# Optimization experiments

Measured on AMD Instinct MI355X. Metric: run time of the kernel, lower is better.

The kernel has to match this reference:

```python
import jax, jax.numpy as jnp
import numpy as np
from jax import lax

KS = 10      # kernel_size (asserted == 10 in the torch module)
DCT_N = 10   # dct_n


def _dct_pair(N):
    k = np.arange(N)[:, None]
    i = np.arange(N)[None, :]
    w = np.full((N, 1), np.sqrt(2.0 / N))
    w[0, 0] = np.sqrt(1.0 / N)
    d = w * np.cos(np.pi * (i + 0.5) * k / N)
    return jnp.asarray(d, jnp.float32), jnp.asarray(np.linalg.inv(d), jnp.float32)


def _conv1d(x, w):
    # x: [B, C, L], w: [O, C, K], VALID conv (bias=False in torch)
    return lax.conv_general_dilated(x, w, (1,), 'VALID',
                                    dimension_numbers=('NCH', 'OIH', 'NCH'))


def _two_conv(x, w1, w2):
    return jax.nn.relu(_conv1d(jax.nn.relu(_conv1d(x, w1)), w2))


def _gconv(x, w, att, b):
    # GraphConvolution: att @ (x @ w) + b ; x: [B, node, f_in]
    return jnp.einsum('nm,bmo->bno', att, jnp.einsum('bmf,fo->bmo', x, w)) + b


def _gcn(x, gc1_w, gc1_att, gc1_b, gcb_w, gcb_att, gcb_b, gc7_w, gc7_att, gc7_b):
    # Standard motion-prediction GCN (eval mode: BN=identity, dropout off)
    y = jnp.tanh(_gconv(x, gc1_w, gc1_att, gc1_b))
    for s in range(gcb_w.shape[0]):  # small fixed num_stage
        h = jnp.tanh(_gconv(y, gcb_w[s, 0], gcb_att[s, 0], gcb_b[s, 0]))
        h = jnp.tanh(_gconv(h, gcb_w[s, 1], gcb_att[s, 1], gcb_b[s, 1]))
        y = y + h
    return _gconv(y, gc7_w, gc7_att, gc7_b) + x


def _ffc(x, wl, wg):
    # RealFFC(dim=3): spectral branch (rFFT over time, 1x1 conv on real/imag,
    # ReLU, irFFT) + local 1x1 branch. x: [B, 3, F/3, T]
    y = jnp.fft.rfft(x, axis=-1)
    yc = jnp.concatenate([y.real, y.imag], axis=1)            # [B, 6, F/3, K]
    yc = jax.nn.relu(jnp.einsum('oc,bcfk->bofk', wg, yc))
    re, im = jnp.split(yc, 2, axis=1)
    spec = jnp.fft.irfft(re + 1j * im, n=x.shape[-1], axis=-1)
    return jnp.einsum('oc,bcft->boft', wl, x) + spec


def _forward(input_seq, wq1, wq2, wk1, wk2,
             gc1_w, gc1_att, gc1_b, gcb_w, gcb_att, gcb_b,
             gc7_w, gc7_att, gc7_b, mlp_w1, mlp_w2, ffc_wl, ffc_wg,
             output_n, input_n):
    seq = input_seq[:, :input_n]
    B, _, F = seq.shape
    blen = KS + output_n                       # DCT block length (30)
    dctm, idctm = _dct_pair(blen)
    key_seq = jnp.swapaxes(seq, 1, 2)[:, :, :input_n - output_n]
    query_seq = jnp.swapaxes(seq, 1, 2)[:, :, -KS:]
    # im2col-style overlapping temporal blocks -> per-block DCT
    nvb = input_n - blen + 1
    idx = np.arange(blen)[None, :] + np.arange(nvb)[:, None]
    blocks = seq[:, idx]                       # [B, nvb, blen, F]
    # matches torch reshape(...,dct_n,-1).transpose(2,3).reshape: feature-major
    dvb = jnp.einsum('dk,bnkf->bnfd', dctm[:DCT_N], blocks).reshape(B, nvb, -1)
    key_feat = _two_conv(key_seq / 1000.0, wk1, wk2)       # [B, D, nvb]
    query_feat = _two_conv(query_seq / 1000.0, wq1, wq2)   # [B, D, 1]
    score = jnp.einsum('bdq,bdk->bqk', query_feat, key_feat) + 1e-15
    attn = score / jnp.sum(score, axis=2, keepdims=True)   # sum-normalized attention
    attended = jnp.einsum('bqk,bkf->bqf', attn, dvb)[:, 0].reshape(B, F, DCT_N)
    # FFC branch: pad with last frame x10, fold F into (3, F//3)
    ffc_in = jnp.concatenate([seq, jnp.repeat(seq[:, -1:], 10, axis=1)], axis=1)
    ffc_in = jnp.swapaxes(ffc_in, 1, 2).reshape(B, 3, F // 3, input_n + 10)
    ffc_out = _ffc(ffc_in, ffc_wl, ffc_wg).reshape(B, F, input_n + 10)[:, :, :DCT_N]
    ffc_out = jnp.swapaxes(ffc_out, 1, 2)      # [B, DCT_N, F]
    # GCN branch: last KS frames + last frame repeated output_n times
    gidx = np.concatenate([np.arange(input_n - KS, input_n),
                           np.full(output_n, input_n - 1)])
    gcn_in = seq[:, gidx]                      # [B, blen, F]
    dct_in = jnp.einsum('dk,bkf->bfd', dctm[:DCT_N], gcn_in)
    gcn_out = _gcn(dct_in, gc1_w, gc1_att, gc1_b, gcb_w, gcb_att, gcb_b,
                   gc7_w, gc7_att, gc7_b)      # [B, F, DCT_N]
    combined = jnp.concatenate([gcn_out, attended], axis=-1)
    recon = jnp.einsum('kd,bfd->bkf', idctm[:, :DCT_N], combined[:, :, :DCT_N])  # [B, blen, F]
    fused = jnp.swapaxes(jnp.concatenate([recon, ffc_out], axis=1), 1, 2)  # [B, F, blen+DCT_N=40]
    h = jax.nn.relu(jnp.einsum('bft,ot->bfo', fused, mlp_w1))  # Linear(40,256), no bias
    out = jnp.einsum('bfo,to->bft', h, mlp_w2)                 # Linear(256,40), no bias
    out = jnp.swapaxes(out, 1, 2)[:, :DCT_N]   # [B, DCT_N, F]
    return out[:, :, None, :]                  # [B, DCT_N, itera=1, F]


def setup_inputs() -> dict:
    key = jax.random.key(0)
    ks = jax.random.split(key, 20)
    B, T, F, D, NS = 1024, 50, 48, 512, 2
    p = lambda k, shp: jax.random.normal(k, shp, dtype=jnp.float32) * 0.05
    return {
        'input_seq': jax.random.normal(ks[0], (B, T, F), dtype=jnp.float32),
        'wq1': p(ks[1], (D, F, 6)), 'wq2': p(ks[2], (D, D, 5)),
        'wk1': p(ks[3], (D, F, 6)), 'wk2': p(ks[4], (D, D, 5)),
        'gc1_w': p(ks[5], (10, D)), 'gc1_att': p(ks[6], (F, F)), 'gc1_b': p(ks[7], (D,)),
        'gcb_w': p(ks[8], (NS, 2, D, D)), 'gcb_att': p(ks[9], (NS, 2, F, F)),
        'gcb_b': p(ks[10], (NS, 2, D)),
        'gc7_w': p(ks[11], (D, 10)), 'gc7_att': p(ks[12], (F, F)), 'gc7_b': p(ks[13], (10,)),
        'mlp_w1': p(ks[14], (256, 40)), 'mlp_w2': p(ks[15], (40, 256)),
        'ffc_wl': p(ks[16], (3, 3)), 'ffc_wg': p(ks[17], (6, 6)),
        'output_n': 20, 'input_n': 50, 'itera': 1,
    }


def reference(input_seq, wq1, wq2, wk1, wk2, gc1_w, gc1_att, gc1_b,
              gcb_w, gcb_att, gcb_b, gc7_w, gc7_att, gc7_b,
              mlp_w1, mlp_w2, ffc_wl, ffc_wg, output_n, input_n, itera):
    assert itera == 1  # single-iteration path (the torch itera>1 branch is skipped)
    return _forward(input_seq, wq1, wq2, wk1, wk2,
                    gc1_w, gc1_att, gc1_b, gcb_w, gcb_att, gcb_b,
                    gc7_w, gc7_att, gc7_b, mlp_w1, mlp_w2, ffc_wl, ffc_wg,
                    output_n, input_n)
```

## Files before the change

### kernel.cpp

```cpp
#include <hip/hip_runtime.h>
#include <math.h>

#define BB 1024
#define TT 50
#define FF 48
#define EXTN 60
#define NFREQ 31

typedef _Float16 h8 __attribute__((ext_vector_type(8)));
typedef _Float16 h4 __attribute__((ext_vector_type(4)));
typedef float f4 __attribute__((ext_vector_type(4)));

__device__ __forceinline__ float fast_tanh(float x) {
    float e = __expf(2.0f * x);
    return 1.0f - 2.0f * __builtin_amdgcn_rcpf(e + 1.0f);
}

__global__ void prep_kernel(const float* __restrict__ gcb_w, _Float16* __restrict__ P,
                            const float* __restrict__ gc1_w, _Float16* __restrict__ P1,
                            const float* __restrict__ gc7_w, _Float16* __restrict__ P7,
                            const float* __restrict__ mlp_w1, _Float16* __restrict__ Pw1,
                            const float* __restrict__ mlp_w2, _Float16* __restrict__ Pw2,
                            const float* __restrict__ gc1_att, const float* __restrict__ gcb_att,
                            const float* __restrict__ gc7_att, _Float16* __restrict__ attp,
                            float* __restrict__ dctm, float* __restrict__ dtail) {
    int blk = blockIdx.x, tid = threadIdx.x;
    const _Float16 HZ = (_Float16)0.0f;
    if (blk < 512) {
        int z = blk >> 7;
        int idx = ((blk & 127) << 8) | tid;
        int lane = idx & 63, t8 = idx >> 6;
        int nt = t8 & 7, kw = t8 >> 3;
        int ks = kw & 15, wv = kw >> 4;
        int n = wv * 128 + nt * 16 + (lane & 15);
        int k0 = ks * 32 + (lane >> 4) * 8;
        const float* src = gcb_w + (size_t)z * 262144 + n;
        h8 v;
        #pragma unroll
        for (int j = 0; j < 8; ++j) v[j] = (_Float16)src[(size_t)(k0 + j) * 512];
        *(h8*)(P + (size_t)z * 262144 + (size_t)idx * 8) = v;
    } else if (blk < 528) {
        int idx = ((blk - 512) << 8) | tid;
        int lane = idx & 63, t8 = idx >> 6;
        int nt = t8 & 7, kw = t8 >> 3;
        int ks = kw & 1, wv = kw >> 1;
        int n = wv * 128 + nt * 16 + (lane & 15);
        int k0 = ks * 32 + (lane >> 4) * 8;
        h8 v;
        #pragma unroll
        for (int j = 0; j < 8; ++j) v[j] = (k0 + j < 10) ? (_Float16)gc1_w[(k0 + j) * 512 + n] : HZ;
        *(h8*)(P1 + (size_t)idx * 8) = v;
    } else if (blk < 532) {
        int idx = ((blk - 528) << 8) | tid;
        int lane = idx & 63, t8 = idx >> 6;
        int ks = t8 & 3, wv = t8 >> 2;
        int n = lane & 15;
        int k0 = wv * 128 + ks * 32 + (lane >> 4) * 8;
        h8 v;
        #pragma unroll
        for (int j = 0; j < 8; ++j) v[j] = (n < 10) ? (_Float16)gc7_w[(k0 + j) * 10 + n] : HZ;
        *(h8*)(P7 + (size_t)idx * 8) = v;
    } else if (blk < 540) {
        int idx = ((blk - 532) << 8) | tid;
        int lane = idx & 63, t8 = idx >> 6;
        int ks = t8 & 1, q = t8 >> 1;
        int nt = q & 3, wv = q >> 2;
        int o = wv * 64 + nt * 16 + (lane & 15);
        int k0 = ks * 32 + (lane >> 4) * 8;
        h8 v;
        #pragma unroll
        for (int j = 0; j < 8; ++j) v[j] = (k0 + j < 40) ? (_Float16)mlp_w1[o * 40 + k0 + j] : HZ;
        *(h8*)(Pw1 + (size_t)idx * 8) = v;
    } else if (blk < 542) {
        int idx = ((blk - 540) << 8) | tid;
        int lane = idx & 63, ks = idx >> 6;
        int m = lane & 15;
        int k0 = ks * 32 + (lane >> 4) * 8;
        h8 v;
        #pragma unroll
        for (int j = 0; j < 8; ++j) v[j] = (m < 10) ? (_Float16)mlp_w2[m * 256 + k0 + j] : HZ;
        *(h8*)(Pw2 + (size_t)idx * 8) = v;
    } else if (blk < 614) {
        int idx = (blk - 542) * 256 + tid;
        if (idx < 18432) {
            int l = idx / 3072, r = (idx % 3072) / 64, m = idx & 63;
            float v = 0.f;
            if (m < 48) {
                v = (l == 0) ? gc1_att[r * 48 + m]
                  : (l <= 4) ? gcb_att[(l - 1) * 2304 + r * 48 + m]
                             : gc7_att[r * 48 + m];
            }
            attp[idx] = (_Float16)v;
        }
    } else {
        int idx = (blk - 614) * 256 + tid;
        if (idx < 900) {
            int d = idx / 30, k = idx % 30;
            double w = (d == 0) ? sqrt(1.0 / 30.0) : sqrt(2.0 / 30.0);
            dctm[idx] = (float)(w * cos(M_PI * (k + 0.5) * d / 30.0));
        } else if (idx < 910) {
            int d = idx - 900;
            double w = (d == 0) ? sqrt(1.0 / 30.0) : sqrt(2.0 / 30.0);
            double s = 0.0;
            for (int k = 10; k < 30; ++k) s += w * cos(M_PI * (k + 0.5) * d / 30.0);
            dtail[d] = (float)s;
        }
    }
}

template<int KSTEPS, int MODE>
__device__ __forceinline__ void gcn_layer(char* S, char* T,
        const _Float16* __restrict__ Pw, const _Float16* __restrict__ attp,
        const float* __restrict__ bias, h4* sv,
        int lane, int wv, int l16, int quad) {
    h8 ab[3][2];
    #pragma unroll
    for (int it = 0; it < 3; ++it)
        #pragma unroll
        for (int ks = 0; ks < 2; ++ks)
            ab[it][ks] = *(const h8*)(attp + (it * 16 + l16) * 64 + ks * 32 + quad * 8);

    f4 acc[3][8];
    #pragma unroll
    for (int mt = 0; mt < 3; ++mt)
        #pragma unroll
        for (int nt = 0; nt < 8; ++nt) acc[mt][nt] = (f4)0.0f;

    const _Float16* Pb = Pw + (size_t)wv * (KSTEPS * 8 * 512) + lane * 8;
    __syncthreads();
    const int xm = l16 & 7;
    #pragma unroll 2
    for (int ks = 0; ks < KSTEPS; ++ks) {
        h8 a[3], bfr[8];
        #pragma unroll
        for (int nt = 0; nt < 8; ++nt)
            bfr[nt] = *(const h8*)(Pb + (ks * 8 + nt) * 512);
        #pragma unroll
        for (int mt = 0; mt < 3; ++mt)
            a[mt] = *(h8*)(S + (mt * 16 + l16) * 1024 + (((ks * 4 + quad) ^ xm) << 4));
        #pragma unroll
        for (int mt = 0; mt < 3; ++mt)
            #pragma unroll
            for (int nt = 0; nt < 8; ++nt)
                acc[mt][nt] = __builtin_amdgcn_mfma_f32_16x16x32_f16(a[mt], bfr[nt], acc[mt][nt], 0, 0, 0);
    }
    __syncthreads();

    if (lane < 48) {
        int row = lane / 3, s = lane % 3;
        *(h8*)(T + row * 144 + 96 + s * 16) = (h8)(_Float16)0.0f;
    }

    #pragma unroll
    for (int nt = 0; nt < 8; ++nt) {
        #pragma unroll
        for (int mt = 0; mt < 3; ++mt) {
            h4 hv;
            #pragma unroll
            for (int j = 0; j < 4; ++j) hv[j] = (_Float16)acc[mt][nt][j];
            *(h4*)(T + l16 * 144 + (mt * 16 + quad * 4) * 2) = hv;
        }
        asm volatile("s_waitcnt lgkmcnt(0)" ::: "memory");
        h8 tf0 = *(h8*)(T + l16 * 144 + quad * 16);
        h8 tf1 = *(h8*)(T + l16 * 144 + 64 + quad * 16);
        f4 acc2[3];
        #pragma unroll
        for (int it = 0; it < 3; ++it) {
            acc2[it] = __builtin_amdgcn_mfma_f32_16x16x32_f16(tf0, ab[it][0], (f4)0.0f, 0, 0, 0);
            acc2[it] = __builtin_amdgcn_mfma_f32_16x16x32_f16(tf1, ab[it][1], acc2[it], 0, 0, 0);
        }
        const int c0 = wv * 128 + nt * 16 + quad * 4;
        const f4 bv = *(const f4*)(bias + c0);
        #pragma unroll
        for (int it = 0; it < 3; ++it) {
            int f = it * 16 + l16;
            char* sp = S + f * 1024 + (((c0 >> 3) ^ (f & 7)) << 4) + ((c0 & 7) << 1);
            if (MODE == 1) sv[nt * 3 + it] = *(h4*)sp;
            h4 o;
            #pragma unroll
            for (int j = 0; j < 4; ++j) {
                float v = fast_tanh(acc2[it][j] + bv[j]);
                if (MODE == 2) v += (float)sv[nt * 3 + it][j];
                o[j] = (_Float16)v;
            }
            *(h4*)sp = o;
        }
    }
}

__launch_bounds__(256, 2)
__global__ void gcn_fused_kernel(const float* __restrict__ seq,
                                 const _Float16* __restrict__ P1,
                                 const _Float16* __restrict__ Pm,
                                 const _Float16* __restrict__ P7,
                                 const _Float16* __restrict__ attp,
                                 const float* __restrict__ gc1_b,
                                 const float* __restrict__ gcb_b,
                                 const float* __restrict__ gc7_b,
                                 const float* __restrict__ dctm,
                                 const float* __restrict__ dtail,
                                 float* __restrict__ fusedb) {
    __shared__ __align__(16) char smem[63744];
    char* S    = smem;
    char* R    = smem + 49152;
    char* dctf = smem + 61440;
    const int tid = threadIdx.x, lane = tid & 63, wv = tid >> 6;
    const int l16 = lane & 15, quad = lane >> 4;
    const int b = blockIdx.x;
    char* T = R + wv * 2304;

    if (tid < 120) *(f4*)(R + tid * 16) = *(const f4*)(seq + (size_t)b * 2400 + 1920 + tid * 4);
    for (int v = tid; v < 310; v += 256)
        ((float*)(R + 2048))[v] = (v < 300) ? dctm[v] : dtail[v - 300];
    __syncthreads();
    for (int v = tid; v < 480; v += 256) {
        int f = v / 10, d = v % 10;
        const float* q = (const float*)R;
        const float* L = (const float*)(R + 2048);
        float a = L[300 + d] * q[9 * 48 + f];
        #pragma unroll
        for (int k = 0; k < 10; ++k) a += L[d * 30 + k] * q[k * 48 + f];
        ((float*)dctf)[f * 12 + d] = a;
    }
    __syncthreads();
    for (int v = tid; v < 384; v += 256) {
        int m = v >> 3, g = v & 7;
        h8 w = (h8)(_Float16)0.0f;
        if (g < 2) {
            #pragma unroll
            for (int j = 0; j < 8; ++j) {
                int d = g * 8 + j;
                if (d < 10) w[j] = (_Float16)((float*)dctf)[m * 12 + d];
            }
        }
        *(h8*)(S + m * 1024 + ((g ^ (m & 7)) << 4)) = w;
    }

    h4 sv[24];
    gcn_layer<2, 0>(S, T, P1,          attp,          gc1_b,        sv, lane, wv, l16, quad);
    gcn_layer<16, 1>(S, T, Pm,          attp + 3072,  gcb_b,        sv, lane, wv, l16, quad);
    gcn_layer<16, 2>(S, T, Pm + 262144, attp + 6144,  gcb_b + 512,  sv, lane, wv, l16, quad);
    gcn_layer<16, 1>(S, T, Pm + 524288, attp + 9216,  gcb_b + 1024, sv, lane, wv, l16, quad);
    gcn_layer<16, 2>(S, T, Pm + 786432, attp + 12288, gcb_b + 1536, sv, lane, wv, l16, quad);

    __syncthreads();
    {
        f4 acc[3];
        #pragma unroll
        for (int mt = 0; mt < 3; ++mt) acc[mt] = (f4)0.0f;
        const _Float16* Pb7 = P7 + wv * 2048 + lane * 8;
        #pragma unroll
        for (int ks = 0; ks < 4; ++ks) {
            h8 bfr = *(const h8*)(Pb7 + ks * 512);
            int kh = wv * 128 + ks * 32;
            #pragma unroll
            for (int mt = 0; mt < 3; ++mt) {
                h8 a = *(h8*)(S + (mt * 16 + l16) * 1024 + ((((kh >> 3) + quad) ^ (l16 & 7)) << 4));
                acc[mt] = __builtin_amdgcn_mfma_f32_16x16x32_f16(a, bfr, acc[mt], 0, 0, 0);
            }
        }
        #pragma unroll
        for (int mt = 0; mt < 3; ++mt)
            *(f4*)(R + wv * 3072 + l16 * 192 + (mt * 16 + quad * 4) * 4) = acc[mt];
    }
    __syncthreads();
    if (wv == 0) {
        h4 tw[3]; int ns[3], ms[3];
        #pragma unroll
        for (int q = 0; q < 3; ++q) {
            int idx = lane * 3 + q;
            int n = idx / 12, m0 = (idx % 12) * 4;
            f4 s = *(f4*)(R + n * 192 + m0 * 4);
            s += *(f4*)(R + 3072 + n * 192 + m0 * 4);
            s += *(f4*)(R + 6144 + n * 192 + m0 * 4);
            s += *(f4*)(R + 9216 + n * 192 + m0 * 4);
            h4 h;
            #pragma unroll
            for (int j = 0; j < 4; ++j) h[j] = (_Float16)s[j];
            tw[q] = h; ns[q] = n; ms[q] = m0;
        }
        asm volatile("s_waitcnt lgkmcnt(0)" ::: "memory");
        #pragma unroll
        for (int q = 0; q < 3; ++q) *(h4*)(R + ns[q] * 144 + ms[q] * 2) = tw[q];
        if (lane < 48) {
            int row = lane / 3, s2 = lane % 3;
            *(h8*)(R + row * 144 + 96 + s2 * 16) = (h8)(_Float16)0.0f;
        }
        asm volatile("s_waitcnt lgkmcnt(0)" ::: "memory");
        h8 tf0 = *(h8*)(R + l16 * 144 + quad * 16);
        h8 tf1 = *(h8*)(R + l16 * 144 + 64 + quad * 16);
        const _Float16* a7 = attp + 15360;
        f4 acc2[3];
        #pragma unroll
        for (int it = 0; it < 3; ++it) {
            h8 ab0 = *(const h8*)(a7 + (it * 16 + l16) * 64 + quad * 8);
            h8 ab1 = *(const h8*)(a7 + (it * 16 + l16) * 64 + 32 + quad * 8);
            acc2[it] = __builtin_amdgcn_mfma_f32_16x16x32_f16(tf0, ab0, (f4)0.0f, 0, 0, 0);
            acc2[it] = __builtin_amdgcn_mfma_f32_16x16x32_f16(tf1, ab1, acc2[it], 0, 0, 0);
        }
        char* G = R + 4096;
        #pragma unroll
        for (int it = 0; it < 3; ++it) {
            int f = it * 16 + l16;
            #pragma unroll
            for (int j = 0; j < 4; ++j) {
                int c = quad * 4 + j;
                if (c < 10) {
                    float v = acc2[it][j] + gc7_b[c] + ((float*)dctf)[f * 12 + c];
                    *(float*)(G + f * 64 + c * 4) = v;
                }
            }
        }
    }
    __syncthreads();
    {
        char* G = R + 4096;
        for (int v = tid; v < 1440; v += 256) {
            int f = v / 30, t = v % 30;
            float s = 0.f;
            #pragma unroll
            for (int d = 0; d < 10; ++d) s += dctm[d * 30 + t] * *(float*)(G + f * 64 + d * 4);
            fusedb[(size_t)b * 1440 + v] = s;
        }
    }
}

__launch_bounds__(256, 3)
__global__ void ffc_mlp_kernel(const float* __restrict__ seq,
                               const float* __restrict__ fusedb,
                               const float* __restrict__ wl,
                               const float* __restrict__ wg,
                               const _Float16* __restrict__ Pw1,
                               const _Float16* __restrict__ Pw2,
                               float* __restrict__ out) {
    __shared__ __align__(16) char smem[45312];
    float* ext = (float*)smem;
    float* Xre = (float*)(smem + 11520);
    float* Xim = (float*)(smem + 17664);
    float* Yo  = (float*)(smem + 23808);
    _Float16* hlds = (_Float16*)smem;
    char* R2 = smem + 25344;
    _Float16* fus = (_Float16*)(smem + 37632);
    float* c60 = (float*)(smem + 44544);
    float* s60 = (float*)(smem + 44784);
    float* wls = (float*)(smem + 45024);
    float* wgs = (float*)(smem + 45072);

    const int b = blockIdx.x, tid = threadIdx.x;
    const int lane = tid & 63, wv = tid >> 6;
    const int l16 = lane & 15, quad = lane >> 4;
    const float* s = seq + (size_t)b * TT * FF;

    for (int idx = tid; idx < EXTN * FF; idx += 256) {
        int t = idx / FF, f = idx % FF;
        int ts = t < TT ? t : TT - 1;
        ext[t * FF + f] = s[ts * FF + f];
    }
    if (tid < 60) { c60[tid] = cospif(tid / 30.0f); s60[tid] = sinpif(tid / 30.0f); }
    if (tid >= 64 && tid < 73) wls[tid - 64] = wl[tid - 64];
    if (tid >= 128 && tid < 164) wgs[tid - 128] = wg[tid - 128];
    __syncthreads();
    for (int idx = tid; idx < FF * NFREQ; idx += 256) {
        int f = idx % FF, k = idx / FF;
        float re = 0.f, im = 0.f;
        int kt = 0;
        for (int t = 0; t < EXTN; ++t) {
            float v = ext[t * FF + f];
            re += v * c60[kt];
            im -= v * s60[kt];
            kt += k; kt = (kt >= 60) ? kt - 60 : kt;
        }
        Xre[f * 32 + k] = re; Xim[f * 32 + k] = im;
    }
    __syncthreads();
    for (int idx = tid; idx < 6 * 16 * NFREQ; idx += 256) {
        int k = idx % NFREQ; int g = (idx / NFREQ) % 16; int o = idx / (NFREQ * 16);
        float v = wgs[o * 6 + 0] * Xre[g * 32 + k]        + wgs[o * 6 + 1] * Xre[(16 + g) * 32 + k]
                + wgs[o * 6 + 2] * Xre[(32 + g) * 32 + k] + wgs[o * 6 + 3] * Xim[g * 32 + k]
                + wgs[o * 6 + 4] * Xim[(16 + g) * 32 + k] + wgs[o * 6 + 5] * Xim[(32 + g) * 32 + k];
        Yo[(o * 16 + g) * 32 + k] = fmaxf(v, 0.f);
    }
    __syncthreads();
    for (int v = tid; v < 1440; v += 256) {
        int f = v / 30, t = v % 30;
        fus[f * 72 + t] = (_Float16)fusedb[(size_t)b * 1440 + v];
    }
    for (int v = tid; v < 1152; v += 256) {
        int f = v / 24, t = 40 + v % 24;
        fus[f * 72 + t] = (_Float16)0.0f;
    }
    for (int idx = tid; idx < 480; idx += 256) {
        int t = idx % 10; int g = (idx / 10) % 16; int c = idx / 160;
        float acc = Yo[(c * 16 + g) * 32 + 0] + Yo[(c * 16 + g) * 32 + 30] * ((t & 1) ? -1.f : 1.f);
        float s2 = 0.f;
        int kt = t;
        for (int k = 1; k < 30; ++k) {
            s2 += Yo[(c * 16 + g) * 32 + k] * c60[kt] - Yo[((c + 3) * 16 + g) * 32 + k] * s60[kt];
            kt += t; kt = (kt >= 60) ? kt - 60 : kt;
        }
        acc = (acc + 2.f * s2) * (1.0f / 60.0f);
        float loc = wls[c * 3 + 0] * ext[t * FF + g] + wls[c * 3 + 1] * ext[t * FF + 16 + g]
                  + wls[c * 3 + 2] * ext[t * FF + 32 + g];
        int f = c * 16 + g;
        fus[f * 72 + 30 + t] = (_Float16)(acc + loc);
    }
    __syncthreads();
    f4 acc1[3][4];
    #pragma unroll
    for (int mt = 0; mt < 3; ++mt)
        #pragma unroll
        for (int nt = 0; nt < 4; ++nt) acc1[mt][nt] = (f4)0.0f;
    #pragma unroll
    for (int ks = 0; ks < 2; ++ks) {
        h8 af[3], bf[4];
        #pragma unroll
        for (int mt = 0; mt < 3; ++mt)
            af[mt] = *(h8*)((char*)fus + (mt * 16 + l16) * 144 + ks * 64 + quad * 16);
        #pragma unroll
        for (int nt = 0; nt < 4; ++nt)
            bf[nt] = *(const h8*)(Pw1 + (size_t)(((wv * 4 + nt) * 2 + ks) * 512) + lane * 8);
        #pragma unroll
        for (int mt = 0; mt < 3; ++mt)
            #pragma unroll
            for (int nt = 0; nt < 4; ++nt)
                acc1[mt][nt] = __builtin_amdgcn_mfma_f32_16x16x32_f16(af[mt], bf[nt], acc1[mt][nt], 0, 0, 0);
    }
    __syncthreads();
    #pragma unroll
    for (int mt = 0; mt < 3; ++mt)
        #pragma unroll
        for (int nt = 0; nt < 4; ++nt) {
            int o = wv * 64 + nt * 16 + l16;
            #pragma unroll
            for (int j = 0; j < 4; ++j) {
                int f = mt * 16 + quad * 4 + j;
                hlds[f * 264 + o] = (_Float16)fmaxf(acc1[mt][nt][j], 0.f);
            }
        }
    __syncthreads();
    f4 acc2[3];
    #pragma unroll
    for (int nt3 = 0; nt3 < 3; ++nt3) acc2[nt3] = (f4)0.0f;
    #pragma unroll
    for (int ss = 0; ss < 2; ++ss) {
        int ks = wv * 2 + ss;
        h8 aw = *(const h8*)(Pw2 + (size_t)ks * 512 + lane * 8);
        #pragma unroll
        for (int nt3 = 0; nt3 < 3; ++nt3) {
            h8 bh = *(h8*)((char*)hlds + (nt3 * 16 + l16) * 528 + ks * 64 + quad * 16);
            acc2[nt3] = __builtin_amdgcn_mfma_f32_16x16x32_f16(aw, bh, acc2[nt3], 0, 0, 0);
        }
    }
    #pragma unroll
    for (int nt3 = 0; nt3 < 3; ++nt3)
        *(f4*)(R2 + wv * 3072 + (nt3 * 16 + l16) * 64 + quad * 16) = acc2[nt3];
    __syncthreads();
    for (int v = tid; v < 768; v += 256) {
        int f = v >> 4, t = v & 15;
        float sm = 0.f;
        #pragma unroll
        for (int w4 = 0; w4 < 4; ++w4) sm += *(float*)(R2 + w4 * 3072 + f * 64 + t * 4);
        if (t < 10) out[(size_t)b * 480 + t * 48 + f] = sm;
    }
}

extern "C" void kernel_launch(void* const* d_in, const int* in_sizes, int n_in,
                              void* d_out, int out_size, void* d_ws, size_t ws_size,
                              hipStream_t stream) {
    (void)in_sizes; (void)n_in; (void)out_size;
    const float* seq     = (const float*)d_in[0];
    const float* gc1_w   = (const float*)d_in[5];
    const float* gc1_att = (const float*)d_in[6];
    const float* gc1_b   = (const float*)d_in[7];
    const float* gcb_w   = (const float*)d_in[8];
    const float* gcb_att = (const float*)d_in[9];
    const float* gcb_b   = (const float*)d_in[10];
    const float* gc7_w   = (const float*)d_in[11];
    const float* gc7_att = (const float*)d_in[12];
    const float* gc7_b   = (const float*)d_in[13];
    const float* mlp_w1  = (const float*)d_in[14];
    const float* mlp_w2  = (const float*)d_in[15];
    const float* ffc_wl  = (const float*)d_in[16];
    const float* ffc_wg  = (const float*)d_in[17];
    float* out = (float*)d_out;
    char* ws = (char*)d_ws;

    float*    dctm  = (float*)ws;
    float*    dtail = dctm + 900;
    char*     p0    = ws + 4096;
    _Float16* Pm   = (_Float16*)p0;   p0 += 4 * 262144 * 2;
    _Float16* P1   = (_Float16*)p0;   p0 += 32768 * 2;
    _Float16* P7   = (_Float16*)p0;   p0 += 8192 * 2;
    _Float16* Pw1  = (_Float16*)p0;   p0 += 16384 * 2;
    _Float16* Pw2  = (_Float16*)p0;   p0 += 4096 * 2;
    _Float16* attp = (_Float16*)p0;   p0 += 18432 * 2;
    const size_t fixed_bytes = (size_t)(p0 - ws);

    const size_t per_batch = 5760;
    size_t avail = (ws_size > fixed_bytes) ? (ws_size - fixed_bytes) : 0;
    int nc = 1;
    while ((size_t)(BB / nc) * per_batch > avail && nc < 64) nc *= 2;
    int Bc = BB / nc;
    float* fusedb = (float*)(ws + fixed_bytes);

    prep_kernel<<<618, 256, 0, stream>>>(gcb_w, Pm, gc1_w, P1, gc7_w, P7,
                                         mlp_w1, Pw1, mlp_w2, Pw2,
                                         gc1_att, gcb_att, gc7_att, attp, dctm, dtail);

    for (int ci = 0; ci < nc; ++ci) {
        const float* seqc = seq + (size_t)ci * Bc * TT * FF;
        float* outc = out + (size_t)ci * Bc * 480;
        gcn_fused_kernel<<<Bc, 256, 0, stream>>>(seqc, P1, Pm, P7, attp,
                                                 gc1_b, gcb_b, gc7_b, dctm, dtail, fusedb);
        ffc_mlp_kernel<<<Bc, 256, 0, stream>>>(seqc, fusedb, ffc_wl, ffc_wg, Pw1, Pw2, outc);
    }
}
```

Measured before the change: 303.7 us.

## Compute FFC forward and inverse DFT with split-fp16 MFMA matrix products

Replaces the scalar per-thread DFT loops in the FFC branch (forward rFFT over 60 samples and the inverse for 10 outputs) with MFMA matrix multiplies. The DFT matrices are precomputed as hi/lo fp16 pairs, and a three-product split keeps accuracy close to fp32. Data is transposed into fp16 hi/lo LDS tiles, which raises shared memory use, so launch bounds drop to 2 blocks per SM. Separately, the attention fragment loads in the GCN layer are moved after the main MFMA loop to lower register pressure.

Result: faster. 284.9 us (-6.2%).

```diff
diff --git a/kernel.cpp b/kernel.cpp
--- a/kernel.cpp
+++ b/kernel.cpp
@@ -23,6 +23,8 @@
                             const float* __restrict__ mlp_w2, _Float16* __restrict__ Pw2,
                             const float* __restrict__ gc1_att, const float* __restrict__ gcb_att,
                             const float* __restrict__ gc7_att, _Float16* __restrict__ attp,
+                            _Float16* __restrict__ Pc_hi, _Float16* __restrict__ Pc_lo,
+                            _Float16* __restrict__ Pi_hi, _Float16* __restrict__ Pi_lo,
                             float* __restrict__ dctm, float* __restrict__ dtail) {
     int blk = blockIdx.x, tid = threadIdx.x;
     const _Float16 HZ = (_Float16)0.0f;
@@ -92,8 +94,36 @@
             }
             attp[idx] = (_Float16)v;
         }
+    } else if (blk < 646) {
+        int g = (blk - 614) * 256 + tid;
+        int tab = g >> 12, e = g & 4095;
+        int j = e & 7, lane = (e >> 3) & 63, t8 = e >> 9;
+        int ks = t8 & 1, nt = t8 >> 1;
+        int n = nt * 16 + (lane & 15);
+        int t = ks * 32 + (lane >> 4) * 8 + j;
+        double v = 0.0;
+        if (t < 60 && n < 62)
+            v = (n < 31) ? cos(M_PI * (double)(n * t) / 30.0)
+                         : -sin(M_PI * (double)((n - 31) * t) / 30.0);
+        _Float16 hi = (_Float16)(float)v;
+        if (tab == 0) Pc_hi[e] = hi;
+        else          Pc_lo[e] = (_Float16)(float)(v - (double)(float)hi);
+    } else if (blk < 654) {
+        int g = (blk - 646) * 256 + tid;
+        int tab = g >> 10, e = g & 1023;
+        int j = e & 7, lane = (e >> 3) & 63, ks = e >> 9;
+        int t = lane & 15;
+        int kp = ks * 32 + (lane >> 4) * 8 + j;
+        double v = 0.0;
+        if (kp == 0) v = 1.0 / 60.0;
+        else if (kp < 30) v = (2.0 / 60.0) * cos(M_PI * (double)(kp * t) / 30.0);
+        else if (kp == 30) v = ((t & 1) ? -1.0 : 1.0) / 60.0;
+        else if (kp >= 32 && kp < 61) v = -(2.0 / 60.0) * sin(M_PI * (double)((kp - 31) * t) / 30.0);
+        _Float16 hi = (_Float16)(float)v;
+        if (tab == 0) Pi_hi[e] = hi;
+        else          Pi_lo[e] = (_Float16)(float)(v - (double)(float)hi);
     } else {
-        int idx = (blk - 614) * 256 + tid;
+        int idx = (blk - 654) * 256 + tid;
         if (idx < 900) {
             int d = idx / 30, k = idx % 30;
             double w = (d == 0) ? sqrt(1.0 / 30.0) : sqrt(2.0 / 30.0);
@@ -113,13 +143,6 @@
         const _Float16* __restrict__ Pw, const _Float16* __restrict__ attp,
         const float* __restrict__ bias, h4* sv,
         int lane, int wv, int l16, int quad) {
-    h8 ab[3][2];
-    #pragma unroll
-    for (int it = 0; it < 3; ++it)
-        #pragma unroll
-        for (int ks = 0; ks < 2; ++ks)
-            ab[it][ks] = *(const h8*)(attp + (it * 16 + l16) * 64 + ks * 32 + quad * 8);
-
     f4 acc[3][8];
     #pragma unroll
     for (int mt = 0; mt < 3; ++mt)
@@ -127,8 +150,9 @@
         for (int nt = 0; nt < 8; ++nt) acc[mt][nt] = (f4)0.0f;
 
     const _Float16* Pb = Pw + (size_t)wv * (KSTEPS * 8 * 512) + lane * 8;
-    __syncthreads();
     const int xm = l16 & 7;
+    __syncthreads();
+
     #pragma unroll 2
     for (int ks = 0; ks < KSTEPS; ++ks) {
         h8 a[3], bfr[8];
@@ -145,6 +169,13 @@
                 acc[mt][nt] = __builtin_amdgcn_mfma_f32_16x16x32_f16(a[mt], bfr[nt], acc[mt][nt], 0, 0, 0);
     }
     __syncthreads();
+
+    h8 ab[3][2];
+    #pragma unroll
+    for (int it = 0; it < 3; ++it)
+        #pragma unroll
+        for (int ks = 0; ks < 2; ++ks)
+            ab[it][ks] = *(const h8*)(attp + (it * 16 + l16) * 64 + ks * 32 + quad * 8);
 
     if (lane < 48) {
         int row = lane / 3, s = lane % 3;
@@ -325,26 +356,31 @@
     }
 }
 
-__launch_bounds__(256, 3)
+__launch_bounds__(256, 2)
 __global__ void ffc_mlp_kernel(const float* __restrict__ seq,
                                const float* __restrict__ fusedb,
                                const float* __restrict__ wl,
                                const float* __restrict__ wg,
                                const _Float16* __restrict__ Pw1,
                                const _Float16* __restrict__ Pw2,
+                               const _Float16* __restrict__ Pc_hi,
+                               const _Float16* __restrict__ Pc_lo,
+                               const _Float16* __restrict__ Pi_hi,
+                               const _Float16* __restrict__ Pi_lo,
                                float* __restrict__ out) {
-    __shared__ __align__(16) char smem[45312];
-    float* ext = (float*)smem;
-    float* Xre = (float*)(smem + 11520);
-    float* Xim = (float*)(smem + 17664);
-    float* Yo  = (float*)(smem + 23808);
+    __shared__ __align__(16) char smem[58560];
+    float* ext     = (float*)smem;
+    char*  extT_hi = smem + 11520;
+    char*  extT_lo = smem + 18432;
+    float* Xre     = (float*)(smem + 25344);
+    float* Xim     = (float*)(smem + 31488);
+    char*  Ya_hi   = smem + 37632;
+    char*  Ya_lo   = smem + 44544;
+    _Float16* fus  = (_Float16*)(smem + 51456);
+    float* wls     = (float*)(smem + 58368);
+    float* wgs     = (float*)(smem + 58404);
     _Float16* hlds = (_Float16*)smem;
-    char* R2 = smem + 25344;
-    _Float16* fus = (_Float16*)(smem + 37632);
-    float* c60 = (float*)(smem + 44544);
-    float* s60 = (float*)(smem + 44784);
-    float* wls = (float*)(smem + 45024);
-    float* wgs = (float*)(smem + 45072);
+    char*  R2      = smem + 25344;
 
     const int b = blockIdx.x, tid = threadIdx.x;
     const int lane = tid & 63, wv = tid >> 6;
@@ -353,34 +389,68 @@
 
     for (int idx = tid; idx < EXTN * FF; idx += 256) {
         int t = idx / FF, f = idx % FF;
-        int ts = t < TT ? t : TT - 1;
-        ext[t * FF + f] = s[ts * FF + f];
-    }
-    if (tid < 60) { c60[tid] = cospif(tid / 30.0f); s60[tid] = sinpif(tid / 30.0f); }
-    if (tid >= 64 && tid < 73) wls[tid - 64] = wl[tid - 64];
-    if (tid >= 128 && tid < 164) wgs[tid - 128] = wg[tid - 128];
-    __syncthreads();
-    for (int idx = tid; idx < FF * NFREQ; idx += 256) {
-        int f = idx % FF, k = idx / FF;
-        float re = 0.f, im = 0.f;
-        int kt = 0;
-        for (int t = 0; t < EXTN; ++t) {
-            float v = ext[t * FF + f];
-            re += v * c60[kt];
-            im -= v * s60[kt];
-            kt += k; kt = (kt >= 60) ? kt - 60 : kt;
-        }
-        Xre[f * 32 + k] = re; Xim[f * 32 + k] = im;
-    }
-    __syncthreads();
-    for (int idx = tid; idx < 6 * 16 * NFREQ; idx += 256) {
-        int k = idx % NFREQ; int g = (idx / NFREQ) % 16; int o = idx / (NFREQ * 16);
+        ext[idx] = s[(t < TT ? t : TT - 1) * FF + f];
+    }
+    for (int idx = tid; idx < 64 * FF; idx += 256) {
+        int t = idx / FF, f = idx % FF;
+        float v = (t < EXTN) ? s[(t < TT ? t : TT - 1) * FF + f] : 0.f;
+        _Float16 hi = (_Float16)v;
+        ((_Float16*)(extT_hi + f * 144))[t] = hi;
+        ((_Float16*)(extT_lo + f * 144))[t] = (_Float16)(v - (float)hi);
+    }
+    if (tid < 9) wls[tid] = wl[tid];
+    if (tid >= 64 && tid < 100) wgs[tid - 64] = wg[tid - 64];
+    __syncthreads();
+
+    {
+        const int nt = wv;
+        f4 acc[3];
+        #pragma unroll
+        for (int mt = 0; mt < 3; ++mt) acc[mt] = (f4)0.0f;
+        #pragma unroll
+        for (int ks = 0; ks < 2; ++ks) {
+            h8 bhi = *(const h8*)(Pc_hi + (nt * 2 + ks) * 512 + lane * 8);
+            h8 blo = *(const h8*)(Pc_lo + (nt * 2 + ks) * 512 + lane * 8);
+            #pragma unroll
+            for (int mt = 0; mt < 3; ++mt) {
+                h8 ahi = *(h8*)(extT_hi + (mt * 16 + l16) * 144 + ks * 64 + quad * 16);
+                h8 alo = *(h8*)(extT_lo + (mt * 16 + l16) * 144 + ks * 64 + quad * 16);
+                acc[mt] = __builtin_amdgcn_mfma_f32_16x16x32_f16(ahi, bhi, acc[mt], 0, 0, 0);
+                acc[mt] = __builtin_amdgcn_mfma_f32_16x16x32_f16(alo, bhi, acc[mt], 0, 0, 0);
+                acc[mt] = __builtin_amdgcn_mfma_f32_16x16x32_f16(ahi, blo, acc[mt], 0, 0, 0);
+            }
+        }
+        int n = nt * 16 + l16;
+        #pragma unroll
+        for (int mt = 0; mt < 3; ++mt)
+            #pragma unroll
+            for (int i = 0; i < 4; ++i) {
+                int f = mt * 16 + quad * 4 + i;
+                if (n < 31) Xre[f * 32 + n] = acc[mt][i];
+                else if (n < 62) Xim[f * 32 + n - 31] = acc[mt][i];
+            }
+    }
+    __syncthreads();
+
+    for (int idx = tid; idx < 2976; idx += 256) {
+        int k = idx % 31; int g = (idx / 31) % 16; int o = idx / (31 * 16);
         float v = wgs[o * 6 + 0] * Xre[g * 32 + k]        + wgs[o * 6 + 1] * Xre[(16 + g) * 32 + k]
                 + wgs[o * 6 + 2] * Xre[(32 + g) * 32 + k] + wgs[o * 6 + 3] * Xim[g * 32 + k]
                 + wgs[o * 6 + 4] * Xim[(16 + g) * 32 + k] + wgs[o * 6 + 5] * Xim[(32 + g) * 32 + k];
-        Yo[(o * 16 + g) * 32 + k] = fmaxf(v, 0.f);
-    }
-    __syncthreads();
+        v = fmaxf(v, 0.f);
+        int fr = (o < 3) ? o * 16 + g : (o - 3) * 16 + g;
+        int kp = (o < 3) ? k : 31 + k;
+        _Float16 hi = (_Float16)v;
+        ((_Float16*)(Ya_hi + fr * 144))[kp] = hi;
+        ((_Float16*)(Ya_lo + fr * 144))[kp] = (_Float16)(v - (float)hi);
+    }
+    if (tid < 96) {
+        int f = tid >> 1, c = 62 + (tid & 1);
+        ((_Float16*)(Ya_hi + f * 144))[c] = (_Float16)0.0f;
+        ((_Float16*)(Ya_lo + f * 144))[c] = (_Float16)0.0f;
+    }
+    __syncthreads();
+
     for (int v = tid; v < 1440; v += 256) {
         int f = v / 30, t = v % 30;
         fus[f * 72 + t] = (_Float16)fusedb[(size_t)b * 1440 + v];
@@ -389,22 +459,34 @@
         int f = v / 24, t = 40 + v % 24;
         fus[f * 72 + t] = (_Float16)0.0f;
     }
-    for (int idx = tid; idx < 480; idx += 256) {
-        int t = idx % 10; int g = (idx / 10) % 16; int c = idx / 160;
-        float acc = Yo[(c * 16 + g) * 32 + 0] + Yo[(c * 16 + g) * 32 + 30] * ((t & 1) ? -1.f : 1.f);
-        float s2 = 0.f;
-        int kt = t;
-        for (int k = 1; k < 30; ++k) {
-            s2 += Yo[(c * 16 + g) * 32 + k] * c60[kt] - Yo[((c + 3) * 16 + g) * 32 + k] * s60[kt];
-            kt += t; kt = (kt >= 60) ? kt - 60 : kt;
-        }
-        acc = (acc + 2.f * s2) * (1.0f / 60.0f);
-        float loc = wls[c * 3 + 0] * ext[t * FF + g] + wls[c * 3 + 1] * ext[t * FF + 16 + g]
-                  + wls[c * 3 + 2] * ext[t * FF + 32 + g];
-        int f = c * 16 + g;
-        fus[f * 72 + 30 + t] = (_Float16)(acc + loc);
-    }
-    __syncthreads();
+    if (wv < 3) {
+        const int mt = wv;
+        f4 ac = (f4)0.0f;
+        #pragma unroll
+        for (int ks = 0; ks < 2; ++ks) {
+            h8 bhi = *(const h8*)(Pi_hi + ks * 512 + lane * 8);
+            h8 blo = *(const h8*)(Pi_lo + ks * 512 + lane * 8);
+            h8 ahi = *(h8*)(Ya_hi + (mt * 16 + l16) * 144 + ks * 64 + quad * 16);
+            h8 alo = *(h8*)(Ya_lo + (mt * 16 + l16) * 144 + ks * 64 + quad * 16);
+            ac = __builtin_amdgcn_mfma_f32_16x16x32_f16(ahi, bhi, ac, 0, 0, 0);
+            ac = __builtin_amdgcn_mfma_f32_16x16x32_f16(alo, bhi, ac, 0, 0, 0);
+            ac = __builtin_amdgcn_mfma_f32_16x16x32_f16(ahi, blo, ac, 0, 0, 0);
+        }
+        int t = l16;
+        if (t < 10) {
+            #pragma unroll
+            for (int i = 0; i < 4; ++i) {
+                int g = quad * 4 + i;
+                int f = mt * 16 + g;
+                float loc = wls[mt * 3 + 0] * ext[t * FF + g]
+                          + wls[mt * 3 + 1] * ext[t * FF + 16 + g]
+                          + wls[mt * 3 + 2] * ext[t * FF + 32 + g];
+                fus[f * 72 + 30 + t] = (_Float16)(ac[i] + loc);
+            }
+        }
+    }
+    __syncthreads();
+
     f4 acc1[3][4];
     #pragma unroll
     for (int mt = 0; mt < 3; ++mt)
@@ -488,12 +570,16 @@
     float*    dctm  = (float*)ws;
     float*    dtail = dctm + 900;
     char*     p0    = ws + 4096;
-    _Float16* Pm   = (_Float16*)p0;   p0 += 4 * 262144 * 2;
-    _Float16* P1   = (_Float16*)p0;   p0 += 32768 * 2;
-    _Float16* P7   = (_Float16*)p0;   p0 += 8192 * 2;
-    _Float16* Pw1  = (_Float16*)p0;   p0 += 16384 * 2;
-    _Float16* Pw2  = (_Float16*)p0;   p0 += 4096 * 2;
-    _Float16* attp = (_Float16*)p0;   p0 += 18432 * 2;
+    _Float16* Pm    = (_Float16*)p0;   p0 += 4 * 262144 * 2;
+    _Float16* P1    = (_Float16*)p0;   p0 += 32768 * 2;
+    _Float16* P7    = (_Float16*)p0;   p0 += 8192 * 2;
+    _Float16* Pw1   = (_Float16*)p0;   p0 += 16384 * 2;
+    _Float16* Pw2   = (_Float16*)p0;   p0 += 4096 * 2;
+    _Float16* attp  = (_Float16*)p0;   p0 += 18432 * 2;
+    _Float16* Pc_hi = (_Float16*)p0;   p0 += 4096 * 2;
+    _Float16* Pc_lo = (_Float16*)p0;   p0 += 4096 * 2;
+    _Float16* Pi_hi = (_Float16*)p0;   p0 += 1024 * 2;
+    _Float16* Pi_lo = (_Float16*)p0;   p0 += 1024 * 2;
     const size_t fixed_bytes = (size_t)(p0 - ws);
 
     const size_t per_batch = 5760;
@@ -503,15 +589,17 @@
     int Bc = BB / nc;
     float* fusedb = (float*)(ws + fixed_bytes);
 
-    prep_kernel<<<618, 256, 0, stream>>>(gcb_w, Pm, gc1_w, P1, gc7_w, P7,
+    prep_kernel<<<658, 256, 0, stream>>>(gcb_w, Pm, gc1_w, P1, gc7_w, P7,
                                          mlp_w1, Pw1, mlp_w2, Pw2,
-                                         gc1_att, gcb_att, gc7_att, attp, dctm, dtail);
+                                         gc1_att, gcb_att, gc7_att, attp,
+                                         Pc_hi, Pc_lo, Pi_hi, Pi_lo, dctm, dtail);
 
     for (int ci = 0; ci < nc; ++ci) {
         const float* seqc = seq + (size_t)ci * Bc * TT * FF;
         float* outc = out + (size_t)ci * Bc * 480;
         gcn_fused_kernel<<<Bc, 256, 0, stream>>>(seqc, P1, Pm, P7, attp,
                                                  gc1_b, gcb_b, gc7_b, dctm, dtail, fusedb);
-        ffc_mlp_kernel<<<Bc, 256, 0, stream>>>(seqc, fusedb, ffc_wl, ffc_wg, Pw1, Pw2, outc);
+        ffc_mlp_kernel<<<Bc, 256, 0, stream>>>(seqc, fusedb, ffc_wl, ffc_wg, Pw1, Pw2,
+                                               Pc_hi, Pc_lo, Pi_hi, Pi_lo, outc);
     }
 }
```
